# Optimization experiments

Measured on AMD Instinct MI355X. Metric: run time of the kernel, lower is better.

The kernel has to match this reference:

```python
import math
import jax, jax.numpy as jnp
import numpy as np

N, H, E, K = 8192, 2048, 8, 2
CF = 1.25


def setup_inputs() -> dict:
    key = jax.random.key(0)
    ks = jax.random.split(key, 5)
    s1 = 1.0 / math.sqrt(H)
    s2 = 1.0 / math.sqrt(2 * H)
    return {
        "tokens": jax.random.normal(ks[0], (N, H), jnp.float32),
        "Wr": jax.random.normal(ks[1], (E, H), jnp.float32) * s1,   # router: logits = x @ Wr.T + br
        "br": jnp.zeros((E,), jnp.float32),
        "W1": jax.random.normal(ks[2], (E, H, 2 * H), jnp.float32) * s1,
        "b1": jnp.zeros((E, 2 * H), jnp.float32),
        "W2": jax.random.normal(ks[3], (E, 2 * H, H), jnp.float32) * s2,
        "b2": jnp.zeros((E, H), jnp.float32),
    }


def reference(tokens, Wr, br, W1, b1, W2, b2):
    n = tokens.shape[0]
    cap = max(1, math.ceil(CF * n / E))  # per-expert capacity (static)

    # --- router + top-k ---
    logits = tokens @ Wr.T + br                         # [N, E]
    scores, expert_ids = jax.lax.top_k(logits, K)       # [N, K]
    probs = jax.nn.softmax(scores, axis=-1)

    # --- flatten dispatches and sort by expert (stable, like the torch code) ---
    flat_e = expert_ids.reshape(-1)                     # [N*K]
    flat_t = jnp.repeat(jnp.arange(n), K)               # [N*K]
    flat_s = probs.reshape(-1).astype(tokens.dtype)     # [N*K]
    order = jnp.argsort(flat_e)                         # jnp.argsort is stable
    se, st, ss = flat_e[order], flat_t[order], flat_s[order]

    # --- capacity-limited gather: fixed [E, cap] index grid ---
    seg_start = jnp.searchsorted(se, jnp.arange(E))     # [E] first slot of each expert segment
    counts = jnp.bincount(se, length=E)                 # [E] tokens routed to each expert
    slot = jnp.arange(cap)
    idx = jnp.clip(seg_start[:, None] + slot[None, :], 0, n * K - 1)  # [E, cap]
    valid = slot[None, :] < jnp.minimum(counts, cap)[:, None]          # [E, cap]
    tok_idx = st[idx]                                   # [E, cap] source token ids
    w = jnp.where(valid, ss[idx], 0.0)[..., None]       # [E, cap, 1] combine weights (0 => dropped)

    # --- grouped per-expert FFN (GEMM over [E, cap, H]) ---
    x = tokens[tok_idx]                                 # [E, cap, H]
    h = jax.nn.gelu(jnp.einsum('ech,ehf->ecf', x, W1) + b1[:, None, :], approximate=False)
    y = jnp.einsum('ecf,efh->ech', h, W2) + b2[:, None, :]

    # --- weighted scatter-add combine ---
    out = jnp.zeros_like(tokens).at[tok_idx.reshape(-1)].add((y * w).reshape(-1, tokens.shape[-1]))
    return out
```

## Files before the change

kernel.cpp:

```cpp
#include <hip/hip_runtime.h>
#include <hip/hip_bf16.h>
#include <math.h>

#define NTOK 8192
#define HDIM 2048
#define NEXP 8
#define TOPK 2
#define CAP  1280
#define FF   4096

typedef float  f32x4  __attribute__((ext_vector_type(4)));
typedef __bf16 bf16x8 __attribute__((ext_vector_type(8)));

typedef __attribute__((address_space(1))) const unsigned int gas_u32;
typedef __attribute__((address_space(3))) unsigned int las_u32;

__device__ __forceinline__ void gload16(const void* g, void* l) {
    __builtin_amdgcn_global_load_lds((gas_u32*)g, (las_u32*)l, 16, 0, 0);
}

__device__ __forceinline__ ushort f2bf(float f) {
    union { float f; unsigned u; } c; c.f = f;
    unsigned u = c.u;
    unsigned r = (u + 0x7FFFu + ((u >> 16) & 1u)) >> 16;
    return (ushort)r;
}
__device__ __forceinline__ float bf2f(ushort h) {
    union { unsigned u; float f; } c; c.u = ((unsigned)h) << 16;
    return c.f;
}

__global__ void k_convert(const float* __restrict__ src, ushort* __restrict__ dst) {
    int i = (blockIdx.x * 256 + threadIdx.x) * 8;
    float4 a = *(const float4*)(src + i);
    float4 b = *(const float4*)(src + i + 4);
    uint4 o;
    o.x = (unsigned)f2bf(a.x) | ((unsigned)f2bf(a.y) << 16);
    o.y = (unsigned)f2bf(a.z) | ((unsigned)f2bf(a.w) << 16);
    o.z = (unsigned)f2bf(b.x) | ((unsigned)f2bf(b.y) << 16);
    o.w = (unsigned)f2bf(b.z) | ((unsigned)f2bf(b.w) << 16);
    *(uint4*)(dst + i) = o;
}

__global__ void k_router(const float* __restrict__ tokens, const float* __restrict__ Wr,
                         const float* __restrict__ br, int* __restrict__ eids,
                         float* __restrict__ probs) {
    int wave = threadIdx.x >> 6, lane = threadIdx.x & 63;
    int t = blockIdx.x * 4 + wave;
    const float* tp = tokens + (size_t)t * HDIM;
    double acc[NEXP];
    #pragma unroll
    for (int e = 0; e < NEXP; ++e) acc[e] = 0.0;
    for (int j = 0; j < HDIM / 64; ++j) {
        float x = tp[j * 64 + lane];
        #pragma unroll
        for (int e = 0; e < NEXP; ++e)
            acc[e] += (double)x * (double)Wr[e * HDIM + j * 64 + lane];
    }
    #pragma unroll
    for (int e = 0; e < NEXP; ++e) {
        #pragma unroll
        for (int off = 32; off; off >>= 1) acc[e] += __shfl_xor(acc[e], off, 64);
    }
    if (lane == 0) {
        float lg[NEXP];
        #pragma unroll
        for (int e = 0; e < NEXP; ++e) lg[e] = (float)acc[e] + br[e];
        int e0 = 0; float s0 = lg[0];
        #pragma unroll
        for (int e = 1; e < NEXP; ++e) if (lg[e] > s0) { s0 = lg[e]; e0 = e; }
        int e1 = -1; float s1 = -1e30f;
        #pragma unroll
        for (int e = 0; e < NEXP; ++e) if (e != e0 && lg[e] > s1) { s1 = lg[e]; e1 = e; }
        float ex = expf(s1 - s0);
        float den = 1.f + ex;
        eids[t * 2] = e0; eids[t * 2 + 1] = e1;
        probs[t * 2] = 1.f / den; probs[t * 2 + 1] = ex / den;
    }
}

__global__ void k_assign(const int* __restrict__ eids, int* __restrict__ tok_map,
                         int* __restrict__ dest) {
    __shared__ int cnt[64][NEXP];
    int l = threadIdx.x;
    for (int i = l; i < NEXP * CAP; i += 64) tok_map[i] = 0;
    int c[NEXP];
    #pragma unroll
    for (int e = 0; e < NEXP; ++e) c[e] = 0;
    const int base = l * 256;
    for (int i = 0; i < 256; ++i) {
        int ee = eids[base + i];
        #pragma unroll
        for (int e = 0; e < NEXP; ++e) c[e] += (ee == e);
    }
    #pragma unroll
    for (int e = 0; e < NEXP; ++e) cnt[l][e] = c[e];
    __syncthreads();
    if (l < NEXP) {
        int run = 0;
        for (int b = 0; b < 64; ++b) { int v = cnt[b][l]; cnt[b][l] = run; run += v; }
    }
    __syncthreads();
    int off[NEXP];
    #pragma unroll
    for (int e = 0; e < NEXP; ++e) off[e] = cnt[l][e];
    for (int i = 0; i < 256; ++i) {
        int d = base + i;
        int ee = eids[d];
        int r = -1;
        #pragma unroll
        for (int e = 0; e < NEXP; ++e) { bool m = (ee == e); if (m) r = off[e]; off[e] += m; }
        if (r < CAP) { tok_map[ee * CAP + r] = d >> 1; dest[d] = ee * CAP + r; }
        else dest[d] = -1;
    }
}

__global__ __launch_bounds__(256) void k_transpose(const float* __restrict__ src,
                                                   ushort* __restrict__ dst,
                                                   int Kd, int Nd) {
    __shared__ float tl[64][65];
    int e = blockIdx.z;
    int k0 = blockIdx.x * 64, n0 = blockIdx.y * 64;
    const float* s = src + (size_t)e * Kd * Nd;
    ushort* d = dst + (size_t)e * Kd * Nd;
    int tid = threadIdx.x;
    #pragma unroll
    for (int i = 0; i < 4; ++i) {
        int flat = (i * 256 + tid) * 4;
        int kk = flat >> 6, nn = flat & 63;
        float4 v = *(const float4*)(s + (size_t)(k0 + kk) * Nd + n0 + nn);
        tl[kk][nn] = v.x; tl[kk][nn + 1] = v.y; tl[kk][nn + 2] = v.z; tl[kk][nn + 3] = v.w;
    }
    __syncthreads();
    #pragma unroll
    for (int g = 0; g < 4; ++g) {
        int flat = g * 1024 + tid * 4;
        int nn = flat >> 6, kk = flat & 63;
        uint2 o;
        o.x = (unsigned)f2bf(tl[kk][nn])     | ((unsigned)f2bf(tl[kk + 1][nn]) << 16);
        o.y = (unsigned)f2bf(tl[kk + 2][nn]) | ((unsigned)f2bf(tl[kk + 3][nn]) << 16);
        *(uint2*)(d + (size_t)(n0 + nn) * Kd + k0 + kk) = o;
    }
}

#define BAR()    __builtin_amdgcn_s_barrier()
#define SCHED0() __builtin_amdgcn_sched_barrier(0)
#define LGKM0()  do { asm volatile("s_waitcnt lgkmcnt(0)" ::: "memory"); SCHED0(); } while (0)
#define VMC4()   do { asm volatile("s_waitcnt vmcnt(4)" ::: "memory"); SCHED0(); } while (0)

template<bool DOGELU, bool GATHER>
__global__ __launch_bounds__(512, 2) void k_gemm(const ushort* __restrict__ A,
                                                 const int* __restrict__ tmap,
                                                 const ushort* __restrict__ B,
                                                 const float* __restrict__ bias,
                                                 ushort* __restrict__ C,
                                                 int Kd, int Nd) {
    __shared__ char lds[131072];
    const int tid  = threadIdx.x;
    const int lane = tid & 63;
    const int wave = tid >> 6;
    const int wr = wave >> 2, wc = wave & 3;
    const int e = blockIdx.z;
    const int bm0 = blockIdx.y * 256, bn0 = blockIdx.x * 256;

    const int srow = tid >> 3;
    const int swzc = (tid ^ (tid >> 3)) & 7;
    const ushort* Be = B + (size_t)e * (size_t)Nd * Kd;
    const ushort* pa[4]; const ushort* pb[4];
    #pragma unroll
    for (int h = 0; h < 2; ++h)
        #pragma unroll
        for (int j = 0; j < 2; ++j) {
            int mrow = bm0 + h * 128 + j * 64 + srow;
            int arow = GATHER ? tmap[e * CAP + mrow] : (e * CAP + mrow);
            pa[h * 2 + j] = A  + (size_t)arow * Kd + swzc * 8;
            pb[h * 2 + j] = Be + (size_t)(bn0 + h * 128 + j * 64 + srow) * Kd + swzc * 8;
        }
    const int ldsW = wave * 1024;

    const int fr = lane & 15, kq = lane >> 4;
    const int x0 = ((kq ^ (fr & 7)) * 16);
    const int sA = wr * 16384 + fr * 128;
    const int sB = 65536 + (wc >> 1) * 16384 + ((wc & 1) * 64 + fr) * 128;

    f32x4  acc[8][4] = {};
    bf16x8 bfr[4][2];

    auto STAGE_A = [&](int b, int kt) {
        #pragma unroll
        for (int hj = 0; hj < 4; ++hj)
            gload16(pa[hj] + (size_t)kt * 64,
                    lds + b * 32768 + (hj >> 1) * 16384 + (hj & 1) * 8192 + ldsW);
    };
    auto STAGE_B = [&](int b, int kt) {
        #pragma unroll
        for (int hj = 0; hj < 4; ++hj)
            gload16(pb[hj] + (size_t)kt * 64,
                    lds + 65536 + b * 32768 + (hj >> 1) * 16384 + (hj & 1) * 8192 + ldsW);
    };
    auto LDA_ = [&](bf16x8 (&af)[4][2], int b, int mh) {
        #pragma unroll
        for (int m = 0; m < 4; ++m)
            #pragma unroll
            for (int ks = 0; ks < 2; ++ks)
                af[m][ks] = *(const bf16x8*)(lds + b * 32768 + sA + (mh * 4 + m) * 2048
                                             + (x0 ^ (ks << 6)));
    };
    auto LDB2 = [&](int b, int nh) {
        #pragma unroll
        for (int n = 0; n < 2; ++n)
            #pragma unroll
            for (int ks = 0; ks < 2; ++ks)
                bfr[nh * 2 + n][ks] = *(const bf16x8*)(lds + b * 32768 + sB
                                                       + (nh * 2 + n) * 2048 + (x0 ^ (ks << 6)));
    };
    auto MMA = [&](bf16x8 (&af)[4][2], int mh, int nh) {
        __builtin_amdgcn_s_setprio(1);
        #pragma unroll
        for (int m = 0; m < 4; ++m)
            #pragma unroll
            for (int n = 0; n < 2; ++n)
                #pragma unroll
                for (int ks = 0; ks < 2; ++ks)
                    acc[mh * 4 + m][nh * 2 + n] = __builtin_amdgcn_mfma_f32_16x16x32_bf16(
                        af[m][ks], bfr[nh * 2 + n][ks], acc[mh * 4 + m][nh * 2 + n], 0, 0, 0);
        __builtin_amdgcn_s_setprio(0);
        SCHED0();
    };

    const int NT  = Kd >> 6;
    const int nt2 = NT >> 1;

    STAGE_A(0, 0); STAGE_B(0, 0); STAGE_B(1, 1);
    VMC4();
    BAR();

    for (int it = 0; it < nt2; ++it) {
        const int kt1  = 2 * it + 1;
        const int ktN  = min(2 * it + 2, NT - 1);
        const int ktN1 = min(2 * it + 3, NT - 1);
        bf16x8 af[4][2];
        LDA_(af, 0, 0); LDB2(0, 0);
        STAGE_A(1, kt1);
        BAR(); LGKM0(); MMA(af, 0, 0); BAR();
        LDB2(0, 1);
        BAR(); LGKM0(); MMA(af, 0, 1); BAR();
        LDA_(af, 0, 1);
        STAGE_B(0, ktN);
        BAR(); LGKM0(); MMA(af, 1, 0); BAR();
        VMC4();
        BAR(); LGKM0(); MMA(af, 1, 1); BAR();
        LDA_(af, 1, 0); LDB2(1, 0);
        STAGE_A(0, ktN);
        BAR(); LGKM0(); MMA(af, 0, 0); BAR();
        LDB2(1, 1);
        BAR(); LGKM0(); MMA(af, 0, 1); BAR();
        LDA_(af, 1, 1);
        STAGE_B(1, ktN1);
        BAR(); LGKM0(); MMA(af, 1, 0); BAR();
        VMC4();
        BAR(); LGKM0(); MMA(af, 1, 1); BAR();
    }

    const float* be = bias + e * Nd;
    ushort* Ce = C + (size_t)e * CAP * Nd;
    const int rl = (lane >> 4) * 4, cl = lane & 15;
    #pragma unroll
    for (int ni = 0; ni < 4; ++ni) {
        int gc = bn0 + wc * 64 + ni * 16 + cl;
        float bv = be[gc];
        #pragma unroll
        for (int mi = 0; mi < 8; ++mi) {
            #pragma unroll
            for (int r = 0; r < 4; ++r) {
                int gr = bm0 + wr * 128 + mi * 16 + rl + r;
                float v = acc[mi][ni][r] + bv;
                if (DOGELU) v = 0.5f * v * (1.f + erff(v * 0.70710678118654752f));
                Ce[(size_t)gr * Nd + gc] = f2bf(v);
            }
        }
    }
}

__global__ void k_combine(const ushort* __restrict__ Y, const int* __restrict__ dest,
                          const float* __restrict__ probs, float* __restrict__ out) {
    int t = blockIdx.x;
    int h0 = threadIdx.x * 8;
    int d0 = dest[t * 2], d1 = dest[t * 2 + 1];
    float p0 = d0 >= 0 ? probs[t * 2] : 0.f;
    float p1 = d1 >= 0 ? probs[t * 2 + 1] : 0.f;
    int r0 = d0 >= 0 ? d0 : 0, r1 = d1 >= 0 ? d1 : 0;
    uint4 a = *(const uint4*)(Y + (size_t)r0 * HDIM + h0);
    uint4 b = *(const uint4*)(Y + (size_t)r1 * HDIM + h0);
    float4 o0, o1;
    o0.x = p0 * bf2f(a.x & 0xffff) + p1 * bf2f(b.x & 0xffff);
    o0.y = p0 * bf2f(a.x >> 16)    + p1 * bf2f(b.x >> 16);
    o0.z = p0 * bf2f(a.y & 0xffff) + p1 * bf2f(b.y & 0xffff);
    o0.w = p0 * bf2f(a.y >> 16)    + p1 * bf2f(b.y >> 16);
    o1.x = p0 * bf2f(a.z & 0xffff) + p1 * bf2f(b.z & 0xffff);
    o1.y = p0 * bf2f(a.z >> 16)    + p1 * bf2f(b.z >> 16);
    o1.z = p0 * bf2f(a.w & 0xffff) + p1 * bf2f(b.w & 0xffff);
    o1.w = p0 * bf2f(a.w >> 16)    + p1 * bf2f(b.w >> 16);
    float* op = out + (size_t)t * HDIM + h0;
    *(float4*)op = o0;
    *(float4*)(op + 4) = o1;
}

extern "C" void kernel_launch(void* const* d_in, const int* in_sizes, int n_in,
                              void* d_out, int out_size, void* d_ws, size_t ws_size,
                              hipStream_t stream) {
    const float* tokens = (const float*)d_in[0];
    const float* Wr     = (const float*)d_in[1];
    const float* br     = (const float*)d_in[2];
    const float* W1     = (const float*)d_in[3];
    const float* b1     = (const float*)d_in[4];
    const float* W2     = (const float*)d_in[5];
    const float* b2     = (const float*)d_in[6];
    float* out = (float*)d_out;
    char* ws = (char*)d_ws;

    int*    eids    = (int*)(ws);
    float*  probs   = (float*)(ws + 65536);
    int*    tok_map = (int*)(ws + 131072);
    int*    dest    = (int*)(ws + 172032);
    size_t off = 1u << 20;
    ushort* TbY = (ushort*)(ws + off);
    off += 41943040;
    ushort* Hm  = (ushort*)(ws + off);
    off += 83886080;
    ushort* WT  = (ushort*)(ws + off);
    (void)in_sizes; (void)n_in; (void)out_size; (void)ws_size;

    k_convert<<<dim3(NTOK * HDIM / 2048), 256, 0, stream>>>(tokens, TbY);
    k_router<<<dim3(NTOK / 4), 256, 0, stream>>>(tokens, Wr, br, eids, probs);
    k_assign<<<dim3(1), 64, 0, stream>>>(eids, tok_map, dest);
    k_transpose<<<dim3(HDIM / 64, FF / 64, NEXP), 256, 0, stream>>>(W1, WT, HDIM, FF);
    k_gemm<true, true><<<dim3(FF / 256, CAP / 256, NEXP), 512, 0, stream>>>(
        TbY, tok_map, WT, b1, Hm, HDIM, FF);
    k_transpose<<<dim3(FF / 64, HDIM / 64, NEXP), 256, 0, stream>>>(W2, WT, FF, HDIM);
    k_gemm<false, false><<<dim3(HDIM / 256, CAP / 256, NEXP), 512, 0, stream>>>(
        Hm, nullptr, WT, b2, TbY, FF, HDIM);
    k_combine<<<dim3(NTOK), 256, 0, stream>>>(TbY, dest, probs, out);
}
```

Measured before the change: 756.5 us.

## Double-buffer MFMA register fragments and use partial lgkmcnt waits in GEMM loop

Splits the A and B register fragments into two banks each (afA/afB, bfX/bfY). The LDS reads for the next quarter-tile are issued before the MFMAs of the current one, and the full lgkmcnt(0) waits become partial waits, so LDS-read latency overlaps matrix math instead of stalling each sub-step. The first fragments are loaded before the loop and refetched at the end of each iteration. This raises VGPR pressure under the 512-thread, 2-block launch bound and could cause spills or lower occupancy.

```diff
diff --git a/kernel.cpp b/kernel.cpp
--- a/kernel.cpp
+++ b/kernel.cpp
@@ -145,7 +145,7 @@
 
 #define BAR()    __builtin_amdgcn_s_barrier()
 #define SCHED0() __builtin_amdgcn_sched_barrier(0)
-#define LGKM0()  do { asm volatile("s_waitcnt lgkmcnt(0)" ::: "memory"); SCHED0(); } while (0)
+#define WAITL(n) do { asm volatile("s_waitcnt lgkmcnt(" #n ")" ::: "memory"); SCHED0(); } while (0)
 #define VMC4()   do { asm volatile("s_waitcnt vmcnt(4)" ::: "memory"); SCHED0(); } while (0)
 
 template<bool DOGELU, bool GATHER>
@@ -184,7 +184,8 @@
     const int sB = 65536 + (wc >> 1) * 16384 + ((wc & 1) * 64 + fr) * 128;
 
     f32x4  acc[8][4] = {};
-    bf16x8 bfr[4][2];
+    bf16x8 afA[4][2], afB[4][2];
+    bf16x8 bfX[2][2], bfY[2][2];
 
     auto STAGE_A = [&](int b, int kt) {
         #pragma unroll
@@ -198,23 +199,23 @@
             gload16(pb[hj] + (size_t)kt * 64,
                     lds + 65536 + b * 32768 + (hj >> 1) * 16384 + (hj & 1) * 8192 + ldsW);
     };
-    auto LDA_ = [&](bf16x8 (&af)[4][2], int b, int mh) {
+    auto LDAq = [&](bf16x8 (&bank)[4][2], int b, int mh) {
         #pragma unroll
         for (int m = 0; m < 4; ++m)
             #pragma unroll
             for (int ks = 0; ks < 2; ++ks)
-                af[m][ks] = *(const bf16x8*)(lds + b * 32768 + sA + (mh * 4 + m) * 2048
-                                             + (x0 ^ (ks << 6)));
-    };
-    auto LDB2 = [&](int b, int nh) {
+                bank[m][ks] = *(const bf16x8*)(lds + b * 32768 + sA + (mh * 4 + m) * 2048
+                                               + (x0 ^ (ks << 6)));
+    };
+    auto LDBq = [&](bf16x8 (&bank)[2][2], int b, int nh) {
         #pragma unroll
         for (int n = 0; n < 2; ++n)
             #pragma unroll
             for (int ks = 0; ks < 2; ++ks)
-                bfr[nh * 2 + n][ks] = *(const bf16x8*)(lds + b * 32768 + sB
-                                                       + (nh * 2 + n) * 2048 + (x0 ^ (ks << 6)));
-    };
-    auto MMA = [&](bf16x8 (&af)[4][2], int mh, int nh) {
+                bank[n][ks] = *(const bf16x8*)(lds + b * 32768 + sB + (nh * 2 + n) * 2048
+                                               + (x0 ^ (ks << 6)));
+    };
+    auto MMAq = [&](bf16x8 (&A4)[4][2], bf16x8 (&B2)[2][2], int mh, int nh) {
         __builtin_amdgcn_s_setprio(1);
         #pragma unroll
         for (int m = 0; m < 4; ++m)
@@ -223,7 +224,7 @@
                 #pragma unroll
                 for (int ks = 0; ks < 2; ++ks)
                     acc[mh * 4 + m][nh * 2 + n] = __builtin_amdgcn_mfma_f32_16x16x32_bf16(
-                        af[m][ks], bfr[nh * 2 + n][ks], acc[mh * 4 + m][nh * 2 + n], 0, 0, 0);
+                        A4[m][ks], B2[n][ks], acc[mh * 4 + m][nh * 2 + n], 0, 0, 0);
         __builtin_amdgcn_s_setprio(0);
         SCHED0();
     };
@@ -234,32 +235,28 @@
     STAGE_A(0, 0); STAGE_B(0, 0); STAGE_B(1, 1);
     VMC4();
     BAR();
+    LDAq(afA, 0, 0); LDBq(bfX, 0, 0);
 
     for (int it = 0; it < nt2; ++it) {
         const int kt1  = 2 * it + 1;
         const int ktN  = min(2 * it + 2, NT - 1);
         const int ktN1 = min(2 * it + 3, NT - 1);
-        bf16x8 af[4][2];
-        LDA_(af, 0, 0); LDB2(0, 0);
-        STAGE_A(1, kt1);
-        BAR(); LGKM0(); MMA(af, 0, 0); BAR();
-        LDB2(0, 1);
-        BAR(); LGKM0(); MMA(af, 0, 1); BAR();
-        LDA_(af, 0, 1);
+        LDBq(bfY, 0, 1); STAGE_A(1, kt1);
+        BAR(); WAITL(4);  MMAq(afA, bfX, 0, 0); BAR();
+        LDAq(afB, 0, 1);
+        BAR(); WAITL(8);  MMAq(afA, bfY, 0, 1); BAR();
         STAGE_B(0, ktN);
-        BAR(); LGKM0(); MMA(af, 1, 0); BAR();
-        VMC4();
-        BAR(); LGKM0(); MMA(af, 1, 1); BAR();
-        LDA_(af, 1, 0); LDB2(1, 0);
-        STAGE_A(0, ktN);
-        BAR(); LGKM0(); MMA(af, 0, 0); BAR();
-        LDB2(1, 1);
-        BAR(); LGKM0(); MMA(af, 0, 1); BAR();
-        LDA_(af, 1, 1);
+        BAR(); WAITL(0);  MMAq(afB, bfX, 1, 0); VMC4(); BAR();
+        LDAq(afA, 1, 0); LDBq(bfX, 1, 0);
+        BAR(); WAITL(12); MMAq(afB, bfY, 1, 1); BAR();
+        LDBq(bfY, 1, 1); STAGE_A(0, ktN);
+        BAR(); WAITL(4);  MMAq(afA, bfX, 0, 0); BAR();
+        LDAq(afB, 1, 1);
+        BAR(); WAITL(8);  MMAq(afA, bfY, 0, 1); BAR();
         STAGE_B(1, ktN1);
-        BAR(); LGKM0(); MMA(af, 1, 0); BAR();
-        VMC4();
-        BAR(); LGKM0(); MMA(af, 1, 1); BAR();
+        BAR(); WAITL(0);  MMAq(afB, bfX, 1, 0); VMC4(); BAR();
+        LDAq(afA, 0, 0); LDBq(bfX, 0, 0);
+        BAR(); WAITL(12); MMAq(afB, bfY, 1, 1); BAR();
     }
 
     const float* be = bias + e * Nd;
```

Measured after the change: 1.096 ms. 1.45x slower.
